# Performance work log

Measured on AMD Instinct MI355X. Metric: run time of the kernel, lower is better.

The kernel has to match this reference:

```python
import jax, jax.numpy as jnp
import numpy as np

EPS = 1e-8

def unit_projection(x):
    # project each embedding vector so its Fourier coefficients have unit magnitude
    f = jnp.fft.fft(x, axis=-1)
    f = f / jnp.maximum(jnp.abs(f), EPS)
    return jnp.real(jnp.fft.ifft(f, axis=-1))

def bind(a, b):
    return jnp.fft.irfft(jnp.fft.rfft(a, axis=-1) * jnp.fft.rfft(b, axis=-1), n=a.shape[-1], axis=-1)

def unbind(s, k):
    # k is unit-magnitude in Fourier domain, so its inverse is its conjugate
    return jnp.fft.irfft(jnp.fft.rfft(s, axis=-1) * jnp.conj(jnp.fft.rfft(k, axis=-1)), n=s.shape[-1], axis=-1)

def layer_norm(x, g, b):
    mu = jnp.mean(x, axis=-1, keepdims=True)
    var = jnp.var(x, axis=-1, keepdims=True)
    return (x - mu) * jax.lax.rsqrt(var + 1e-5) * g + b

def setup_inputs():
    key = jax.random.key(0)
    ks = jax.random.split(key, 12)
    B, S, D = 4, 2048, 1024
    sc = 1.0 / np.sqrt(D)
    inp = {
        'x': jax.random.normal(ks[0], (B, S, D), jnp.float32),
        'Wq': jax.random.normal(ks[1], (D, D), jnp.float32) * sc,
        'bq': jnp.zeros((D,), jnp.float32),
        'Wk': jax.random.normal(ks[2], (D, D), jnp.float32) * sc,
        'bk': jnp.zeros((D,), jnp.float32),
        'Wv': jax.random.normal(ks[3], (D, D), jnp.float32) * sc,
        'bv': jnp.zeros((D,), jnp.float32),
        'ln1_g': jnp.ones((D,), jnp.float32), 'ln1_b': jnp.zeros((D,), jnp.float32),
        'ln2_g': jnp.ones((D,), jnp.float32), 'ln2_b': jnp.zeros((D,), jnp.float32),
        'W1': jax.random.normal(ks[4], (D, 4 * D), jnp.float32) * sc,
        'b1': jnp.zeros((4 * D,), jnp.float32),
        'W2': jax.random.normal(ks[5], (4 * D, D), jnp.float32) * (1.0 / np.sqrt(4 * D)),
        'b2': jnp.zeros((D,), jnp.float32),
    }
    return inp

def reference(x, Wq, bq, Wk, bk, Wv, bv, ln1_g, ln1_b, ln2_g, ln2_b, W1, b1, W2, b2):
    h = layer_norm(x, ln1_g, ln1_b)
    q = unit_projection(h @ Wq + bq)
    k = unit_projection(h @ Wk + bk)
    v = unit_projection(h @ Wv + bv)
    s = jnp.cumsum(bind(k, v), axis=1)  # causal prefix-sum over sequence
    mixed = unbind(s, q)
    x = x + mixed  # dropout=0.0
    h2 = layer_norm(x, ln2_g, ln2_b)
    mlp = jax.nn.gelu(h2 @ W1 + b1, approximate=False) @ W2 + b2
    return x + mlp
```

## Files before the change

### kernel.cpp

```cpp
#include <hip/hip_runtime.h>
#include <cstdint>
#include <cstddef>

#define DD 1024
#define SSEQ 2048
#define NB 4
#define MROWS 8192
#define FBINS 513
#define FPAD 520
#define WFP 1152
#define NQKV 3456
#define NHID 4096
#define NCHUNK 64
#define SCHUNK 32

typedef _Float16 f16_t;
typedef _Float16 f16x8 __attribute__((ext_vector_type(8)));
typedef _Float16 f16x2 __attribute__((ext_vector_type(2)));
typedef float f32x4 __attribute__((ext_vector_type(4)));

__device__ __forceinline__ float2 cmul(float2 a, float2 b) {
  return make_float2(a.x * b.x - a.y * b.y, a.x * b.y + a.y * b.x);
}

__device__ __forceinline__ void async_cp16(const void* g, void* l) {
  __builtin_amdgcn_global_load_lds(
      (const __attribute__((address_space(1))) void*)g,
      (__attribute__((address_space(3))) void*)l, 16, 0, 0);
}

template <int N> __device__ __forceinline__ void vwait();
template <> __device__ __forceinline__ void vwait<0>() { asm volatile("s_waitcnt vmcnt(0)" ::: "memory"); }
template <> __device__ __forceinline__ void vwait<1>() { asm volatile("s_waitcnt vmcnt(1)" ::: "memory"); }
template <> __device__ __forceinline__ void vwait<2>() { asm volatile("s_waitcnt vmcnt(2)" ::: "memory"); }
template <> __device__ __forceinline__ void vwait<3>() { asm volatile("s_waitcnt vmcnt(3)" ::: "memory"); }
template <> __device__ __forceinline__ void vwait<4>() { asm volatile("s_waitcnt vmcnt(4)" ::: "memory"); }

__device__ __forceinline__ float fast_gelu(float val) {
  float av = __builtin_fabsf(val);
  float z = av * 0.70710678118654752f;
  float t = __builtin_amdgcn_rcpf(__builtin_fmaf(0.3275911f, z, 1.0f));
  float poly = t * __builtin_fmaf(t,
      __builtin_fmaf(t, __builtin_fmaf(t,
          __builtin_fmaf(t, 1.061405429f, -1.453152027f),
          1.421413741f), -0.284496736f), 0.254829592f);
  float e = __builtin_amdgcn_exp2f(z * z * -1.4426950408889634f);
  float w = poly * e;
  float r = fmaxf(val, 0.0f);
  return __builtin_fmaf(-0.5f * av, w, r);
}

__device__ __forceinline__ void fft1024(float2* bufA, float2* bufB,
                                        const float2* tw, int lt) {
  float2* s = bufA;
  float2* d = bufB;
  for (int m = 1; m < 1024; m <<= 1) {
#pragma unroll
    for (int r2 = 0; r2 < 2; ++r2) {
      int u = lt + r2 * 256;
      int k = u & (m - 1);
      int jm = u - k;
      float2 c0 = s[u];
      float2 c1 = s[u + 512];
      float2 wt = tw[jm];
      float2 su = make_float2(c0.x + c1.x, c0.y + c1.y);
      float2 df = make_float2(c0.x - c1.x, c0.y - c1.y);
      float2 pr = cmul(wt, df);
      d[2 * jm + k] = su;
      d[2 * jm + k + m] = pr;
    }
    __syncthreads();
    float2* tmp = s; s = d; d = tmp;
  }
}

__device__ __forceinline__ float2* fft512(float2* bufA, float2* bufB,
                                          const float2* tw, int lt) {
  float2* s = bufA;
  float2* d = bufB;
  for (int m = 1; m < 512; m <<= 1) {
    int u = lt;
    int k = u & (m - 1);
    int jm = u - k;
    float2 c0 = s[u];
    float2 c1 = s[u + 256];
    float2 wt = tw[jm];
    float2 su = make_float2(c0.x + c1.x, c0.y + c1.y);
    float2 df = make_float2(c0.x - c1.x, c0.y - c1.y);
    float2 pr = cmul(wt, df);
    d[2 * jm + k] = su;
    d[2 * jm + k + m] = pr;
    __syncthreads();
    float2* tmp = s; s = d; d = tmp;
  }
  return s;
}

__global__ __launch_bounds__(512) void wfft_k(
    const float* __restrict__ Wq, const float* __restrict__ Wk,
    const float* __restrict__ Wv, float* __restrict__ WfAll) {
  __shared__ float2 tw[512];
  __shared__ float2 bufA[2][1024];
  __shared__ float2 bufB[2][1024];
  const int tid = threadIdx.x;
  const int rh = tid >> 8;
  const int lt = tid & 255;
  const int row = blockIdx.x * 2 + rh;
  const int p = row >> 10, k = row & 1023;
  const float* W = (p == 0) ? Wq : ((p == 1) ? Wk : Wv);
  if (rh == 0) {
    for (int t = lt; t < 512; t += 256) {
      float ang = -6.2831853071795864769f * (float)t * (1.0f / 1024.0f);
      tw[t] = make_float2(cosf(ang), sinf(ang));
    }
  }
  const float* src = W + (size_t)k * DD;
  for (int t = lt; t < 1024; t += 256) bufA[rh][t] = make_float2(src[t], 0.f);
  __syncthreads();
  fft1024(bufA[rh], bufB[rh], tw, lt);
  float* dst = WfAll + ((size_t)p * DD + k) * WFP;
  for (int t = lt; t <= 512; t += 256) {
    float2 f = bufA[rh][t];
    dst[2 * t] = f.x;
    dst[2 * t + 1] = f.y;
  }
  for (int j = 1026 + lt; j < WFP; j += 256) dst[j] = 0.f;
}

__global__ __launch_bounds__(256) void bfft_k(
    const float* __restrict__ bq, const float* __restrict__ bk,
    const float* __restrict__ bv, float* __restrict__ biasC) {
  __shared__ float2 tw[512];
  __shared__ float2 bufA[1024];
  __shared__ float2 bufB[1024];
  const int tid = threadIdx.x;
  const int p = blockIdx.x;
  const float* bsrc = (p == 0) ? bq : ((p == 1) ? bk : bv);
  for (int t = tid; t < 512; t += 256) {
    float ang = -6.2831853071795864769f * (float)t * (1.0f / 1024.0f);
    tw[t] = make_float2(cosf(ang), sinf(ang));
  }
  for (int t = tid; t < 1024; t += 256) bufA[t] = make_float2(bsrc[t], 0.f);
  __syncthreads();
  fft1024(bufA, bufB, tw, tid);
  float* dst = biasC + (size_t)p * WFP;
  for (int t = tid; t <= 512; t += 256) {
    float2 f = bufA[t];
    dst[2 * t] = f.x;
    dst[2 * t + 1] = f.y;
  }
  for (int j = 1026 + tid; j < WFP; j += 256) dst[j] = 0.f;
}

__global__ __launch_bounds__(256) void transpose_cast_k(
    const float* __restrict__ W, f16_t* __restrict__ Wt, int K, int N) {
  __shared__ float tile[32][33];
  const int tx = threadIdx.x & 31, ty = threadIdx.x >> 5;
  const int n0 = blockIdx.x * 32, k0 = blockIdx.y * 32;
#pragma unroll
  for (int i = 0; i < 32; i += 8)
    tile[ty + i][tx] = W[(size_t)(k0 + ty + i) * N + n0 + tx];
  __syncthreads();
#pragma unroll
  for (int i = 0; i < 32; i += 8)
    Wt[(size_t)(n0 + ty + i) * K + k0 + tx] = (f16_t)tile[tx][ty + i];
}

__global__ __launch_bounds__(256) void ln_cast2_k(
    const float* __restrict__ x, const float* __restrict__ g,
    const float* __restrict__ b, f16_t* __restrict__ hH,
    f16_t* __restrict__ hL) {
  const int row = blockIdx.x, tid = threadIdx.x;
  __shared__ float red[8];
  const float* xr = x + (size_t)row * DD;
  float v[4], ls = 0.f, lq = 0.f;
#pragma unroll
  for (int i = 0; i < 4; ++i) {
    v[i] = xr[i * 256 + tid];
    ls += v[i];
    lq += v[i] * v[i];
  }
#pragma unroll
  for (int o = 32; o > 0; o >>= 1) {
    ls += __shfl_down(ls, o);
    lq += __shfl_down(lq, o);
  }
  const int lane = tid & 63, w = tid >> 6;
  if (lane == 0) { red[w] = ls; red[w + 4] = lq; }
  __syncthreads();
  const float S = red[0] + red[1] + red[2] + red[3];
  const float Q = red[4] + red[5] + red[6] + red[7];
  const float mean = S * (1.f / 1024.f);
  const float var = Q * (1.f / 1024.f) - mean * mean;
  const float rs = rsqrtf(var + 1e-5f);
#pragma unroll
  for (int i = 0; i < 4; ++i) {
    int n = i * 256 + tid;
    float val = (v[i] - mean) * rs * g[n] + b[n];
    f16_t hi = (f16_t)val;
    hH[(size_t)row * DD + n] = hi;
    hL[(size_t)row * DD + n] = (f16_t)(val - (float)hi);
  }
}

template <int RHALF>
__device__ __forceinline__ void stage_half(const f16_t* __restrict__ G,
                                           int grow0, int ldk, int kt,
                                           f16_t* ls, int w, int lane) {
  const int srow = lane >> 3;
  const int slot = lane & 7;
#pragma unroll
  for (int j = 0; j < RHALF / 64; ++j) {
    const int rb = (w + j * 8) * 8;
    const int row = rb + srow;
    const int gg = (slot - (row & 7)) & 7;
    async_cp16(G + (size_t)(grow0 + row) * ldk + kt + gg * 8, ls + rb * 64);
  }
}

template <int BM, int BN>
__device__ __forceinline__ void readA(const f16_t* As, int mq, int wm, int lane,
                                      f16x8 (&aR)[BM / 64][2]) {
#pragma unroll
  for (int mf = 0; mf < BM / 64; ++mf) {
    const int m = mq * (BM / 2) + wm * (BM / 4) + mf * 16 + (lane & 15);
#pragma unroll
    for (int ks = 0; ks < 2; ++ks) {
      const int cg = ks * 4 + (lane >> 4);
      const int sl = (cg + (m & 7)) & 7;
      aR[mf][ks] = *(const f16x8*)(As + m * 64 + sl * 8);
    }
  }
}

template <int BM, int BN>
__device__ __forceinline__ void readB(const f16_t* Bs, int nq, int wn, int lane,
                                      f16x8 (&bR)[BN / 128][2]) {
#pragma unroll
  for (int nf = 0; nf < BN / 128; ++nf) {
    const int n = nq * (BN / 2) + wn * (BN / 8) + nf * 16 + (lane & 15);
#pragma unroll
    for (int ks = 0; ks < 2; ++ks) {
      const int cg = ks * 4 + (lane >> 4);
      const int sl = (cg + (n & 7)) & 7;
      bR[nf][ks] = *(const f16x8*)(Bs + n * 64 + sl * 8);
    }
  }
}

template <int MF, int NF>
__device__ __forceinline__ void mfma_q(f32x4 (&acc)[MF][NF],
                                       const f16x8 (&aR)[MF][2],
                                       const f16x8 (&bR)[NF][2]) {
#pragma unroll
  for (int ks = 0; ks < 2; ++ks)
#pragma unroll
    for (int mf = 0; mf < MF; ++mf)
#pragma unroll
      for (int nf = 0; nf < NF; ++nf)
        acc[mf][nf] = __builtin_amdgcn_mfma_f32_16x16x32_f16(
            aR[mf][ks], bR[nf][ks], acc[mf][nf], 0, 0, 0);
}

template <int BM, int BN, int MM, int NN, int KK, int EPI>
__global__ __launch_bounds__(512, 2) void gemm8p_k(
    const f16_t* __restrict__ A, const f16_t* __restrict__ Bt,
    const float* __restrict__ bias, const float* __restrict__ resid,
    float* __restrict__ outF, f16_t* __restrict__ outH) {
  constexpr int MF = BM / 64;
  constexpr int NF = BN / 128;
  constexpr int LA = BM / 128;
  constexpr int LB = BN / 128;
  constexpr int NT = KK / 64;
  constexpr int TILE = (BM + BN) * 64;
  __shared__ alignas(16) f16_t lds[2 * TILE];

  const int tid = threadIdx.x;
  const int lane = tid & 63;
  const int w = tid >> 6;
  const int wm = w >> 2;
  const int wn = w & 3;

  constexpr int ntm = MM / BM, ntn = NN / BN;
  constexpr int per = (ntm * ntn) / 8;
  const int lin = (int)blockIdx.x;
  const int s = (lin & 7) * per + (lin >> 3);
  const int bn = (s % ntn) * BN;
  const int bm = (s / ntn) * BM;

  f32x4 acc[2][2][MF][NF];
#pragma unroll
  for (int a0 = 0; a0 < 2; ++a0)
#pragma unroll
    for (int a1 = 0; a1 < 2; ++a1)
#pragma unroll
      for (int mf = 0; mf < MF; ++mf)
#pragma unroll
        for (int nf = 0; nf < NF; ++nf)
          acc[a0][a1][mf][nf] = (f32x4){0.f, 0.f, 0.f, 0.f};

  {
    f16_t* A0s = lds;
    f16_t* B0s = lds + BM * 64;
    stage_half<BM / 2>(A, bm, KK, 0, A0s, w, lane);
    stage_half<BN / 2>(Bt, bn, KK, 0, B0s, w, lane);
    stage_half<BN / 2>(Bt, bn + BN / 2, KK, 0, B0s + (BN / 2) * 64, w, lane);
    stage_half<BM / 2>(A, bm + BM / 2, KK, 0, A0s + (BM / 2) * 64, w, lane);
  }
  vwait<LA + LB>();
  __builtin_amdgcn_s_barrier();

  f16x8 aR[MF][2], bR0[NF][2], bR1[NF][2];

  for (int t = 0; t < NT; ++t) {
    const int cur = t & 1;
    f16_t* As = lds + cur * TILE;
    f16_t* Bs = As + BM * 64;
    f16_t* Asn = lds + (cur ^ 1) * TILE;
    f16_t* Bsn = Asn + BM * 64;
    const bool pre = (t + 1 < NT);
    const int ktn = (t + 1) << 6;

    readA<BM, BN>(As, 0, wm, lane, aR);
    readB<BM, BN>(Bs, 0, wn, lane, bR0);
    if (pre) stage_half<BM / 2>(A, bm, KK, ktn, Asn, w, lane);
    __builtin_amdgcn_s_barrier();
    __builtin_amdgcn_s_setprio(1);
    mfma_q<MF, NF>(acc[0][0], aR, bR0);
    __builtin_amdgcn_s_setprio(0);
    if (pre) vwait<2 * LA>(); else vwait<LA>();
    __builtin_amdgcn_s_barrier();

    readB<BM, BN>(Bs, 1, wn, lane, bR1);
    if (pre) stage_half<BN / 2>(Bt, bn, KK, ktn, Bsn, w, lane);
    __builtin_amdgcn_s_barrier();
    __builtin_amdgcn_s_setprio(1);
    mfma_q<MF, NF>(acc[0][1], aR, bR1);
    __builtin_amdgcn_s_setprio(0);
    if (pre) vwait<LA + LB>(); else vwait<0>();
    __builtin_amdgcn_s_barrier();

    readA<BM, BN>(As, 1, wm, lane, aR);
    if (pre) stage_half<BN / 2>(Bt, bn + BN / 2, KK, ktn,
                                Bsn + (BN / 2) * 64, w, lane);
    __builtin_amdgcn_s_barrier();
    __builtin_amdgcn_s_setprio(1);
    mfma_q<MF, NF>(acc[1][0], aR, bR0);
    __builtin_amdgcn_s_setprio(0);
    __builtin_amdgcn_s_barrier();

    if (pre) stage_half<BM / 2>(A, bm + BM / 2, KK, ktn,
                                Asn + (BM / 2) * 64, w, lane);
    __builtin_amdgcn_s_barrier();
    __builtin_amdgcn_s_setprio(1);
    mfma_q<MF, NF>(acc[1][1], aR, bR1);
    __builtin_amdgcn_s_setprio(0);
    if (pre) vwait<LA + LB>();
    __builtin_amdgcn_s_barrier();
  }

  const int q4 = lane >> 4;
  const int cn = lane & 15;
#pragma unroll
  for (int mq = 0; mq < 2; ++mq)
#pragma unroll
    for (int nq = 0; nq < 2; ++nq)
#pragma unroll
      for (int mf = 0; mf < MF; ++mf)
#pragma unroll
        for (int nf = 0; nf < NF; ++nf) {
          const int gcol = bn + nq * (BN / 2) + wn * (BN / 8) + nf * 16 + cn;
          const float bv = bias[gcol];
          const int grow0 = bm + mq * (BM / 2) + wm * (BM / 4) + mf * 16 + q4 * 4;
#pragma unroll
          for (int i = 0; i < 4; ++i) {
            const float val = acc[mq][nq][mf][nf][i] + bv;
            const size_t idx = (size_t)(grow0 + i) * NN + gcol;
            if (EPI == 1) {
              outH[idx] = (f16_t)fast_gelu(val);
            } else {
              outF[idx] = val + resid[idx];
            }
          }
        }
}

__global__ __launch_bounds__(512, 2) void gemm_qkv8p_k(
    const f16_t* __restrict__ Ahi, const f16_t* __restrict__ Alo,
    const f16_t* __restrict__ Bt, const float* __restrict__ bias,
    float* __restrict__ outF) {
  constexpr int BM = 256, BN = 128;
  constexpr int MF = 4, NF = 1;
  constexpr int TILE = (BM + BN) * 64;
  __shared__ alignas(16) f16_t lds[2 * TILE];

  const int tid = threadIdx.x;
  const int lane = tid & 63;
  const int w = tid >> 6;
  const int wm = w >> 2, wn = w & 3;

  const int lin = (int)blockIdx.x;
  const int xcd = lin & 7, idx = lin >> 3;
  int bm, bn;
  bool qmode;
  if (idx < 36) {
    const int h = xcd * 36 + idx;
    bm = (h / 9) * 256;
    bn = (h % 9) * 128;
    qmode = true;
  } else {
    const int l = xcd * 72 + (idx - 36);
    bm = (l / 18) * 256;
    bn = 1152 + (l % 18) * 128;
    qmode = false;
  }
  const int NT = qmode ? 32 : 16;

  f32x4 acc[2][2][MF][NF];
#pragma unroll
  for (int a0 = 0; a0 < 2; ++a0)
#pragma unroll
    for (int a1 = 0; a1 < 2; ++a1)
#pragma unroll
      for (int mf = 0; mf < MF; ++mf)
#pragma unroll
        for (int nf = 0; nf < NF; ++nf)
          acc[a0][a1][mf][nf] = (f32x4){0.f, 0.f, 0.f, 0.f};

  stage_half<128>(Ahi, bm, DD, 0, lds, w, lane);
  stage_half<128>(Bt, bn, DD, 0, lds + BM * 64, w, lane);
  stage_half<128>(Ahi, bm + 128, DD, 0, lds + 128 * 64, w, lane);
  vwait<2>();
  __builtin_amdgcn_s_barrier();

  f16x8 aR[MF][2], bR0[NF][2], bR1[NF][2];

  for (int t = 0; t < NT; ++t) {
    const int cur = t & 1;
    f16_t* As = lds + cur * TILE;
    f16_t* Bs = As + BM * 64;
    f16_t* Asn = lds + (cur ^ 1) * TILE;
    f16_t* Bsn = Asn + BM * 64;
    const bool pre = (t + 1 < NT);
    const int tt = t + 1;
    const f16_t* An = (qmode && tt >= 16) ? Alo : Ahi;
    const int ktn = (tt & 15) << 6;

    readA<BM, BN>(As, 0, wm, lane, aR);
    readB<BM, BN>(Bs, 0, wn, lane, bR0);
    readB<BM, BN>(Bs, 1, wn, lane, bR1);
    if (pre) {
      stage_half<128>(An, bm, DD, ktn, Asn, w, lane);
      stage_half<128>(Bt, bn, DD, ktn, Bsn, w, lane);
    }
    __builtin_amdgcn_s_barrier();
    __builtin_amdgcn_s_setprio(1);
    mfma_q<MF, NF>(acc[0][0], aR, bR0);
    mfma_q<MF, NF>(acc[0][1], aR, bR1);
    __builtin_amdgcn_s_setprio(0);
    if (pre) vwait<4>(); else vwait<0>();
    __builtin_amdgcn_s_barrier();

    readA<BM, BN>(As, 1, wm, lane, aR);
    if (pre) stage_half<128>(An, bm + 128, DD, ktn, Asn + 128 * 64, w, lane);
    __builtin_amdgcn_s_barrier();
    __builtin_amdgcn_s_setprio(1);
    mfma_q<MF, NF>(acc[1][0], aR, bR0);
    mfma_q<MF, NF>(acc[1][1], aR, bR1);
    __builtin_amdgcn_s_setprio(0);
    if (pre) vwait<2>();
    __builtin_amdgcn_s_barrier();
  }

  const int q4 = lane >> 4;
  const int cn = lane & 15;
#pragma unroll
  for (int mq = 0; mq < 2; ++mq)
#pragma unroll
    for (int nq = 0; nq < 2; ++nq)
#pragma unroll
      for (int mf = 0; mf < MF; ++mf)
#pragma unroll
        for (int nf = 0; nf < NF; ++nf) {
          const int gcol = bn + nq * (BN / 2) + wn * (BN / 8) + nf * 16 + cn;
          const float bv = bias[gcol];
          const int grow0 = bm + mq * (BM / 2) + wm * (BM / 4) + mf * 16 + q4 * 4;
#pragma unroll
          for (int i = 0; i < 4; ++i) {
            const size_t oidx = (size_t)(grow0 + i) * NQKV + gcol;
            outF[oidx] = acc[mq][nq][mf][nf][i] + bv;
          }
        }
}

__device__ __forceinline__ float2 unitc(float2 a) {
  float inv = 1.0f / fmaxf(sqrtf(a.x * a.x + a.y * a.y), 1e-8f);
  return make_float2(a.x * inv, a.y * inv);
}
__device__ __forceinline__ float2 bind_bin(const float2* r, int f) {
  float2 kn = unitc(r[576 + f]);
  float2 vn = unitc(r[1152 + f]);
  return cmul(kn, vn);
}

__global__ __launch_bounds__(256) void scan_pass1_k(
    const float* __restrict__ qkvF, float2* __restrict__ T) {
  const int bid = blockIdx.x;
  const int sc = bid & 63;
  const int fh = (bid >> 6) & 1;
  const int b = bid >> 7;
  const int s0 = sc * SCHUNK;
  const float2* base = (const float2*)(qkvF + ((size_t)(b * SSEQ + s0)) * NQKV);
  for (int f = fh * 256 + threadIdx.x; f < FBINS; f += 512) {
    float2 acc = make_float2(0.f, 0.f);
    const float2* r = base;
    for (int i = 0; i < SCHUNK; ++i) {
      float2 pv = bind_bin(r, f);
      acc.x += pv.x; acc.y += pv.y;
      r += NQKV / 2;
    }
    T[((size_t)b * NCHUNK + sc) * FBINS + f] = acc;
  }
}

__global__ void scan_pass2_k(float2* __restrict__ T) {
  const int idx = blockIdx.x * 256 + threadIdx.x;
  if (idx >= NB * FBINS) return;
  const int b = idx / FBINS, f = idx % FBINS;
  float2 acc = make_float2(0.f, 0.f);
  for (int sc = 0; sc < NCHUNK; ++sc) {
    size_t a = ((size_t)b * NCHUNK + sc) * FBINS + f;
    float2 v = T[a];
    T[a] = acc;
    acc.x += v.x; acc.y += v.y;
  }
}

__global__ __launch_bounds__(256) void scan_pass3_k(
    const float* __restrict__ qkvF, const float2* __restrict__ T,
    float2* __restrict__ Scum) {
  const int bid = blockIdx.x;
  const int sc = bid & 63;
  const int fh = (bid >> 6) & 1;
  const int b = bid >> 7;
  const int s0 = sc * SCHUNK;
  const float2* base = (const float2*)(qkvF + ((size_t)(b * SSEQ + s0)) * NQKV);
  for (int f = fh * 256 + threadIdx.x; f < FBINS; f += 512) {
    float2 acc = T[((size_t)b * NCHUNK + sc) * FBINS + f];
    const float2* r = base;
    size_t orow = ((size_t)(b * SSEQ + s0)) * FPAD + f;
    for (int i = 0; i < SCHUNK; ++i) {
      float2 pv = bind_bin(r, f);
      acc.x += pv.x; acc.y += pv.y;
      Scum[orow] = acc;
      r += NQKV / 2;
      orow += FPAD;
    }
  }
}

__global__ __launch_bounds__(512) void unbind_ln2_k(
    const float2* __restrict__ Scum, const float* __restrict__ qkvF,
    const float* __restrict__ x, float* __restrict__ x2out,
    f16_t* __restrict__ h2, const float* __restrict__ g2,
    const float* __restrict__ b2) {
  __shared__ float2 tw[256];
  __shared__ float2 Marr[2][513];
  __shared__ float2 bufA[2][512];
  __shared__ float2 bufB[2][512];
  __shared__ float red[2][8];
  const int tid = threadIdx.x;
  const int rh = tid >> 8;
  const int lt = tid & 255;
  const int row = blockIdx.x * 2 + rh;

  if (rh == 0) {
    float ang = 6.2831853071795864769f * (float)lt * (1.0f / 512.0f);
    tw[lt] = make_float2(cosf(ang), sinf(ang));
  }
  const float2* qrow = (const float2*)(qkvF + (size_t)row * NQKV);
  for (int t = lt; t <= 512; t += 256) {
    float2 sc = Scum[(size_t)row * FPAD + t];
    float2 fq = unitc(qrow[t]);
    Marr[rh][t] = make_float2(sc.x * fq.x + sc.y * fq.y,
                              sc.y * fq.x - sc.x * fq.y);
  }
  __syncthreads();
#pragma unroll
  for (int rr = 0; rr < 2; ++rr) {
    int t = lt + rr * 256;
    float2 a = Marr[rh][t];
    float2 b = Marr[rh][512 - t];
    float2 E = make_float2(0.5f * (a.x + b.x), 0.5f * (a.y - b.y));
    float2 Dd = make_float2(0.5f * (a.x - b.x), 0.5f * (a.y + b.y));
    float ang = 6.2831853071795864769f * (float)t * (1.0f / 1024.0f);
    float cw = cosf(ang), sw = sinf(ang);
    float2 O = make_float2(cw * Dd.x - sw * Dd.y, cw * Dd.y + sw * Dd.x);
    bufA[rh][t] = make_float2(E.x - O.y, E.y + O.x);
  }
  __syncthreads();
  float2* res = fft512(bufA[rh], bufB[rh], tw, lt);

  const float* xr = x + (size_t)row * DD;
  float v[2][2];
  float ls = 0.f, lq = 0.f;
#pragma unroll
  for (int rr = 0; rr < 2; ++rr) {
    int n = lt + rr * 256;
    float2 z = res[n];
    float2 xv = *(const float2*)(xr + 2 * n);
    float v0 = xv.x + z.x * (1.0f / 512.0f);
    float v1 = xv.y + z.y * (1.0f / 512.0f);
    *(float2*)(x2out + (size_t)row * DD + 2 * n) = make_float2(v0, v1);
    v[rr][0] = v0; v[rr][1] = v1;
    ls += v0 + v1;
    lq += v0 * v0 + v1 * v1;
  }
#pragma unroll
  for (int o = 32; o > 0; o >>= 1) {
    ls += __shfl_down(ls, o);
    lq += __shfl_down(lq, o);
  }
  const int lane = tid & 63, w4 = (tid >> 6) & 3;
  if (lane == 0) { red[rh][w4] = ls; red[rh][w4 + 4] = lq; }
  __syncthreads();
  const float S = red[rh][0] + red[rh][1] + red[rh][2] + red[rh][3];
  const float Q = red[rh][4] + red[rh][5] + red[rh][6] + red[rh][7];
  const float mean = S * (1.f / 1024.f);
  const float var = Q * (1.f / 1024.f) - mean * mean;
  const float rs = rsqrtf(var + 1e-5f);
  f16_t* hr = h2 + (size_t)row * DD;
#pragma unroll
  for (int rr = 0; rr < 2; ++rr) {
    int n = lt + rr * 256;
    float2 gv = *(const float2*)(g2 + 2 * n);
    float2 bv = *(const float2*)(b2 + 2 * n);
    f16x2 hp;
    hp[0] = (f16_t)((v[rr][0] - mean) * rs * gv.x + bv.x);
    hp[1] = (f16_t)((v[rr][1] - mean) * rs * gv.y + bv.y);
    *(f16x2*)(hr + 2 * n) = hp;
  }
}

extern "C" void kernel_launch(void* const* d_in, const int* in_sizes, int n_in,
                              void* d_out, int out_size, void* d_ws,
                              size_t ws_size, hipStream_t stream) {
  const float* x     = (const float*)d_in[0];
  const float* Wq    = (const float*)d_in[1];
  const float* bq    = (const float*)d_in[2];
  const float* Wk    = (const float*)d_in[3];
  const float* bk    = (const float*)d_in[4];
  const float* Wv    = (const float*)d_in[5];
  const float* bv    = (const float*)d_in[6];
  const float* ln1_g = (const float*)d_in[7];
  const float* ln1_b = (const float*)d_in[8];
  const float* ln2_g = (const float*)d_in[9];
  const float* ln2_b = (const float*)d_in[10];
  const float* W1    = (const float*)d_in[11];
  const float* b1    = (const float*)d_in[12];
  const float* W2    = (const float*)d_in[13];
  const float* b2    = (const float*)d_in[14];
  float* out = (float*)d_out;

  char* p = (char*)d_ws;
  auto take = [&](size_t bytes) {
    char* r = p;
    p += (bytes + 255) & ~(size_t)255;
    return r;
  };
  f16_t* BtH   = (f16_t*)take((size_t)NQKV * DD * sizeof(f16_t));
  f16_t* W1T   = (f16_t*)take((size_t)NHID * DD * sizeof(f16_t));
  f16_t* W2T   = (f16_t*)take((size_t)DD * NHID * sizeof(f16_t));
  float* biasC = (float*)take((size_t)NQKV * sizeof(float));
  f16_t* hbuf  = (f16_t*)take((size_t)MROWS * DD * sizeof(f16_t));
  char*  big   = take((size_t)MROWS * NQKV * sizeof(float));
  float2* Scum = (float2*)take((size_t)MROWS * FPAD * sizeof(float2));
  float* x2    = (float*)take((size_t)MROWS * DD * sizeof(float));
  float2* Tch  = (float2*)take((size_t)NB * NCHUNK * FBINS * sizeof(float2));
  float* WfAll   = (float*)big;
  float* qkv_f   = (float*)big;
  f16_t* mlp1    = (f16_t*)big;
  f16_t* hlo     = (f16_t*)x2;

  wfft_k<<<3 * DD / 2, 512, 0, stream>>>(Wq, Wk, Wv, WfAll);
  for (int pp = 0; pp < 3; ++pp)
    transpose_cast_k<<<dim3(WFP / 32, DD / 32), 256, 0, stream>>>(
        WfAll + (size_t)pp * DD * WFP,
        BtH + (size_t)pp * WFP * DD, DD, WFP);
  bfft_k<<<3, 256, 0, stream>>>(bq, bk, bv, biasC);
  transpose_cast_k<<<dim3(128, 32), 256, 0, stream>>>(W1, W1T, DD, NHID);
  transpose_cast_k<<<dim3(32, 128), 256, 0, stream>>>(W2, W2T, NHID, DD);

  ln_cast2_k<<<MROWS, 256, 0, stream>>>(x, ln1_g, ln1_b, hbuf, hlo);

  gemm_qkv8p_k<<<864, 512, 0, stream>>>(hbuf, hlo, BtH, biasC, qkv_f);

  scan_pass1_k<<<NB * NCHUNK * 2, 256, 0, stream>>>(qkv_f, Tch);
  scan_pass2_k<<<(NB * FBINS + 255) / 256, 256, 0, stream>>>(Tch);
  scan_pass3_k<<<NB * NCHUNK * 2, 256, 0, stream>>>(qkv_f, Tch, Scum);

  unbind_ln2_k<<<MROWS / 2, 512, 0, stream>>>(Scum, qkv_f, x, x2, hbuf,
                                              ln2_g, ln2_b);

  gemm8p_k<256, 256, MROWS, NHID, DD, 1><<<512, 512, 0, stream>>>(
      hbuf, W1T, b1, nullptr, nullptr, mlp1);

  gemm8p_k<128, 256, MROWS, DD, NHID, 2><<<256, 512, 0, stream>>>(
      mlp1, W2T, b2, x2, out, nullptr);
}
```

Baseline: 518.2 us.

## Drop hi/lo split fp16 for Q projection and use simpler QKV GEMM

Layer norm 1 now writes only a single fp16 copy instead of hi and lo halves. The QKV projection no longer runs a second K pass over the low part for the Q columns. The double-buffered 256x128 GEMM with priority hints is replaced by a simpler single-buffered 128x128 tile kernel with an XCD-aware block remap. This removes about a quarter of the QKV matrix FLOPs and one fp16 output stream. In exchange it loses accuracy on Q, whose unit projection is sensitive to error, and loses the load/compute overlap of the old kernel.

```diff
diff --git a/kernel.cpp b/kernel.cpp
--- a/kernel.cpp
+++ b/kernel.cpp
@@ -166,10 +166,9 @@
     Wt[(size_t)(n0 + ty + i) * K + k0 + tx] = (f16_t)tile[tx][ty + i];
 }
 
-__global__ __launch_bounds__(256) void ln_cast2_k(
+__global__ __launch_bounds__(256) void ln_cast_k(
     const float* __restrict__ x, const float* __restrict__ g,
-    const float* __restrict__ b, f16_t* __restrict__ hH,
-    f16_t* __restrict__ hL) {
+    const float* __restrict__ b, f16_t* __restrict__ hH) {
   const int row = blockIdx.x, tid = threadIdx.x;
   __shared__ float red[8];
   const float* xr = x + (size_t)row * DD;
@@ -197,9 +196,91 @@
   for (int i = 0; i < 4; ++i) {
     int n = i * 256 + tid;
     float val = (v[i] - mean) * rs * g[n] + b[n];
-    f16_t hi = (f16_t)val;
-    hH[(size_t)row * DD + n] = hi;
-    hL[(size_t)row * DD + n] = (f16_t)(val - (float)hi);
+    hH[(size_t)row * DD + n] = (f16_t)val;
+  }
+}
+
+__global__ __launch_bounds__(256, 3) void gemm_qkv_k(
+    const f16_t* __restrict__ A, const f16_t* __restrict__ Bt,
+    const float* __restrict__ bias, float* __restrict__ outF) {
+  __shared__ alignas(16) f16_t AsH[128 * 64];
+  __shared__ alignas(16) f16_t BsH[128 * 64];
+  const int tid = threadIdx.x;
+  const int lane = tid & 63;
+  const int w = tid >> 6;
+  const int wm = w >> 1, wn = w & 1;
+
+  const int lin = blockIdx.x;
+  const int s = (lin & 7) * 216 + (lin >> 3);
+  const int g = s / 108;
+  const int r = s % 108;
+  const int n = r >> 2;
+  const int m0 = g * 4 + (r & 3);
+  const int bn = n * 128;
+  const int bm = m0 * 128;
+
+  f32x4 acc[4][4];
+#pragma unroll
+  for (int i = 0; i < 4; ++i)
+#pragma unroll
+    for (int j = 0; j < 4; ++j) acc[i][j] = (f32x4){0.f, 0.f, 0.f, 0.f};
+
+  const int srow = lane >> 3;
+  const int slot = lane & 7;
+
+  for (int kt = 0; kt < 1024; kt += 64) {
+#pragma unroll
+    for (int i = 0; i < 4; ++i) {
+      const int rb = (i * 4 + w) * 8;
+      const int row = rb + srow;
+      const int gg = (slot - (row & 7)) & 7;
+      size_t ga = (size_t)(bm + row) * 1024 + kt + gg * 8;
+      size_t gb = (size_t)(bn + row) * 1024 + kt + gg * 8;
+      async_cp16(A + ga, &AsH[rb * 64]);
+      async_cp16(Bt + gb, &BsH[rb * 64]);
+    }
+    __syncthreads();
+#pragma unroll
+    for (int ks = 0; ks < 2; ++ks) {
+      const int cgbase = ks * 4 + (lane >> 4);
+      f16x8 ah[4], bh[4];
+#pragma unroll
+      for (int mt = 0; mt < 4; ++mt) {
+        int m = wm * 64 + mt * 16 + (lane & 15);
+        int sl = (cgbase + (m & 7)) & 7;
+        ah[mt] = *(const f16x8*)(&AsH[m * 64 + sl * 8]);
+      }
+#pragma unroll
+      for (int nt = 0; nt < 4; ++nt) {
+        int nn = wn * 64 + nt * 16 + (lane & 15);
+        int sl = (cgbase + (nn & 7)) & 7;
+        bh[nt] = *(const f16x8*)(&BsH[nn * 64 + sl * 8]);
+      }
+#pragma unroll
+      for (int mt = 0; mt < 4; ++mt)
+#pragma unroll
+        for (int nt = 0; nt < 4; ++nt)
+          acc[mt][nt] = __builtin_amdgcn_mfma_f32_16x16x32_f16(
+              ah[mt], bh[nt], acc[mt][nt], 0, 0, 0);
+    }
+    __syncthreads();
+  }
+
+  const int q = lane >> 4;
+  const int cn = lane & 15;
+#pragma unroll
+  for (int mt = 0; mt < 4; ++mt) {
+#pragma unroll
+    for (int nt = 0; nt < 4; ++nt) {
+      const int gcol = bn + wn * 64 + nt * 16 + cn;
+      const float bv = bias[gcol];
+      const int grow0 = bm + wm * 64 + mt * 16 + q * 4;
+#pragma unroll
+      for (int i = 0; i < 4; ++i) {
+        size_t idx = (size_t)(grow0 + i) * NQKV + gcol;
+        outF[idx] = acc[mt][nt][i] + bv;
+      }
+    }
   }
 }
 
@@ -381,114 +462,6 @@
             } else {
               outF[idx] = val + resid[idx];
             }
-          }
-        }
-}
-
-__global__ __launch_bounds__(512, 2) void gemm_qkv8p_k(
-    const f16_t* __restrict__ Ahi, const f16_t* __restrict__ Alo,
-    const f16_t* __restrict__ Bt, const float* __restrict__ bias,
-    float* __restrict__ outF) {
-  constexpr int BM = 256, BN = 128;
-  constexpr int MF = 4, NF = 1;
-  constexpr int TILE = (BM + BN) * 64;
-  __shared__ alignas(16) f16_t lds[2 * TILE];
-
-  const int tid = threadIdx.x;
-  const int lane = tid & 63;
-  const int w = tid >> 6;
-  const int wm = w >> 2, wn = w & 3;
-
-  const int lin = (int)blockIdx.x;
-  const int xcd = lin & 7, idx = lin >> 3;
-  int bm, bn;
-  bool qmode;
-  if (idx < 36) {
-    const int h = xcd * 36 + idx;
-    bm = (h / 9) * 256;
-    bn = (h % 9) * 128;
-    qmode = true;
-  } else {
-    const int l = xcd * 72 + (idx - 36);
-    bm = (l / 18) * 256;
-    bn = 1152 + (l % 18) * 128;
-    qmode = false;
-  }
-  const int NT = qmode ? 32 : 16;
-
-  f32x4 acc[2][2][MF][NF];
-#pragma unroll
-  for (int a0 = 0; a0 < 2; ++a0)
-#pragma unroll
-    for (int a1 = 0; a1 < 2; ++a1)
-#pragma unroll
-      for (int mf = 0; mf < MF; ++mf)
-#pragma unroll
-        for (int nf = 0; nf < NF; ++nf)
-          acc[a0][a1][mf][nf] = (f32x4){0.f, 0.f, 0.f, 0.f};
-
-  stage_half<128>(Ahi, bm, DD, 0, lds, w, lane);
-  stage_half<128>(Bt, bn, DD, 0, lds + BM * 64, w, lane);
-  stage_half<128>(Ahi, bm + 128, DD, 0, lds + 128 * 64, w, lane);
-  vwait<2>();
-  __builtin_amdgcn_s_barrier();
-
-  f16x8 aR[MF][2], bR0[NF][2], bR1[NF][2];
-
-  for (int t = 0; t < NT; ++t) {
-    const int cur = t & 1;
-    f16_t* As = lds + cur * TILE;
-    f16_t* Bs = As + BM * 64;
-    f16_t* Asn = lds + (cur ^ 1) * TILE;
-    f16_t* Bsn = Asn + BM * 64;
-    const bool pre = (t + 1 < NT);
-    const int tt = t + 1;
-    const f16_t* An = (qmode && tt >= 16) ? Alo : Ahi;
-    const int ktn = (tt & 15) << 6;
-
-    readA<BM, BN>(As, 0, wm, lane, aR);
-    readB<BM, BN>(Bs, 0, wn, lane, bR0);
-    readB<BM, BN>(Bs, 1, wn, lane, bR1);
-    if (pre) {
-      stage_half<128>(An, bm, DD, ktn, Asn, w, lane);
-      stage_half<128>(Bt, bn, DD, ktn, Bsn, w, lane);
-    }
-    __builtin_amdgcn_s_barrier();
-    __builtin_amdgcn_s_setprio(1);
-    mfma_q<MF, NF>(acc[0][0], aR, bR0);
-    mfma_q<MF, NF>(acc[0][1], aR, bR1);
-    __builtin_amdgcn_s_setprio(0);
-    if (pre) vwait<4>(); else vwait<0>();
-    __builtin_amdgcn_s_barrier();
-
-    readA<BM, BN>(As, 1, wm, lane, aR);
-    if (pre) stage_half<128>(An, bm + 128, DD, ktn, Asn + 128 * 64, w, lane);
-    __builtin_amdgcn_s_barrier();
-    __builtin_amdgcn_s_setprio(1);
-    mfma_q<MF, NF>(acc[1][0], aR, bR0);
-    mfma_q<MF, NF>(acc[1][1], aR, bR1);
-    __builtin_amdgcn_s_setprio(0);
-    if (pre) vwait<2>();
-    __builtin_amdgcn_s_barrier();
-  }
-
-  const int q4 = lane >> 4;
-  const int cn = lane & 15;
-#pragma unroll
-  for (int mq = 0; mq < 2; ++mq)
-#pragma unroll
-    for (int nq = 0; nq < 2; ++nq)
-#pragma unroll
-      for (int mf = 0; mf < MF; ++mf)
-#pragma unroll
-        for (int nf = 0; nf < NF; ++nf) {
-          const int gcol = bn + nq * (BN / 2) + wn * (BN / 8) + nf * 16 + cn;
-          const float bv = bias[gcol];
-          const int grow0 = bm + mq * (BM / 2) + wm * (BM / 4) + mf * 16 + q4 * 4;
-#pragma unroll
-          for (int i = 0; i < 4; ++i) {
-            const size_t oidx = (size_t)(grow0 + i) * NQKV + gcol;
-            outF[oidx] = acc[mq][nq][mf][nf][i] + bv;
           }
         }
 }
@@ -680,7 +653,6 @@
   float* WfAll   = (float*)big;
   float* qkv_f   = (float*)big;
   f16_t* mlp1    = (f16_t*)big;
-  f16_t* hlo     = (f16_t*)x2;
 
   wfft_k<<<3 * DD / 2, 512, 0, stream>>>(Wq, Wk, Wv, WfAll);
   for (int pp = 0; pp < 3; ++pp)
@@ -691,9 +663,10 @@
   transpose_cast_k<<<dim3(128, 32), 256, 0, stream>>>(W1, W1T, DD, NHID);
   transpose_cast_k<<<dim3(32, 128), 256, 0, stream>>>(W2, W2T, NHID, DD);
 
-  ln_cast2_k<<<MROWS, 256, 0, stream>>>(x, ln1_g, ln1_b, hbuf, hlo);
-
-  gemm_qkv8p_k<<<864, 512, 0, stream>>>(hbuf, hlo, BtH, biasC, qkv_f);
+  ln_cast_k<<<MROWS, 256, 0, stream>>>(x, ln1_g, ln1_b, hbuf);
+
+  gemm_qkv_k<<<(NQKV / 128) * (MROWS / 128), 256, 0, stream>>>(
+      hbuf, BtH, biasC, qkv_f);
 
   scan_pass1_k<<<NB * NCHUNK * 2, 256, 0, stream>>>(qkv_f, Tch);
   scan_pass2_k<<<(NB * FBINS + 255) / 256, 256, 0, stream>>>(Tch);
```

New measurement: 476.0 us. 8.1% less time.
